# Kernel tuning notes

Measured on AMD Instinct MI355X. Metric: run time of the kernel, lower is better.

Reference implementation:

```python
import jax, jax.numpy as jnp
import numpy as np

D = 768        # word_emb_dim * 3 (span embedding dim)
H = 1024       # assumed FFNNScore hidden width
K = 250        # antecedent window (self.k)
P_LAMBDA = 0.4


def setup_inputs() -> dict:
    key = jax.random.key(0)
    ks = jax.random.split(key, 8)
    N, T = 2000, 1000
    return {
        "vectors": jax.random.normal(ks[0], (N, D), jnp.float32),
        "Wm1": jax.random.normal(ks[1], (D, H), jnp.float32) / np.sqrt(D),
        "bm1": jnp.zeros((H,), jnp.float32),
        "wm2": jax.random.normal(ks[2], (H,), jnp.float32) / np.sqrt(H),
        "bm2": jnp.zeros((1,), jnp.float32),
        "Wp1": jax.random.normal(ks[3], (3 * D, H), jnp.float32) / np.sqrt(3 * D),
        "bp1": jnp.zeros((H,), jnp.float32),
        "wp2": jax.random.normal(ks[4], (H,), jnp.float32) / np.sqrt(H),
        "bp2": jnp.zeros((1,), jnp.float32),
        "span_starts": jax.random.randint(ks[5], (N,), 0, T, dtype=jnp.int32),
        "span_ends": jax.random.randint(ks[6], (N,), 0, T, dtype=jnp.int32),
        "t": T,
    }


def reference(vectors, Wm1, bm1, wm2, bm2, Wp1, bp1, wp2, bp2,
              span_starts, span_ends, t):
    m = int(P_LAMBDA * t)  # number of retained spans (static)

    # mention scorer: FFNN over all span embeddings  [N]
    scores = jax.nn.relu(vectors @ Wm1 + bm1) @ wm2 + bm2[0]

    # prune to top int(p_lambda * t) spans by mention score (descending sort)
    top = jnp.argsort(-scores)[:m]
    s_top, v_top = scores[top], vectors[top]

    # re-sort retained spans by (i_start, i_end) descending
    order = jnp.lexsort((span_ends[top], span_starts[top]))[::-1]
    v, s = v_top[order], s_top[order]  # [m, D], [m]

    # pairwise scorer weight split for cat([a, b, a*b]) @ Wp1
    Wa, Wb, Wab = Wp1[:D], Wp1[D:2 * D], Wp1[2 * D:]

    # antecedent windows: span i vs spans i+1 .. i+K (padded/masked)
    idx = jnp.arange(m - 1)[:, None] + 1 + jnp.arange(K)[None, :]  # [m-1, K]
    valid = idx < m
    idxc = jnp.minimum(idx, m - 1)

    a = v[:m - 1]                      # [m-1, D]
    b = v[idxc]                        # [m-1, K, D]
    hb = (v @ Wb)[idxc]                # gather precomputed b-projection [m-1, K, H]
    h = jax.nn.relu((a @ Wa)[:, None, :] + hb
                    + jnp.einsum('ikd,dh->ikh', a[:, None, :] * b, Wab)
                    + bp1)             # [m-1, K, H]
    pairwise = h @ wp2 + bp2[0]        # [m-1, K]

    ant = pairwise + s[idxc] + s[:m - 1, None]
    ant = jnp.where(valid, ant, -jnp.inf)
    # dummy antecedent (epsilon) score 0 appended, then softmax per span
    full = jnp.concatenate([ant, jnp.zeros((m - 1, 1), ant.dtype)], axis=1)
    return jax.nn.softmax(full, axis=-1)  # [m-1, K+1]
```

## Files before the change

### kernel.cpp

```cpp
#include <hip/hip_runtime.h>
#include <hip/hip_bf16.h>
#include <math.h>

#define NVEC 2000
#define DD   768
#define HH   1024
#define KNUM 250
#define MSEL 400
#define MR   399
#define OUTW 251
#define PPAD 256
#define NPAIR (MR * PPAD)
#define BM 128
#define BN 256
#define BK 64
#define NKT (DD / BK)
#define NNB (HH / BN)

typedef short  bf16x8 __attribute__((ext_vector_type(8)));
typedef float  f32x4  __attribute__((ext_vector_type(4)));
typedef unsigned int u32;
typedef u32    u32x4  __attribute__((ext_vector_type(4)));

__device__ __forceinline__ float waveSum(float p) {
#pragma unroll
  for (int off = 32; off >= 1; off >>= 1) p += __shfl_xor(p, off, 64);
  return p;
}
__device__ __forceinline__ float waveMax(float p) {
#pragma unroll
  for (int off = 32; off >= 1; off >>= 1) p = fmaxf(p, __shfl_xor(p, off, 64));
  return p;
}
__device__ __forceinline__ short f2bf(float f) {
  __hip_bfloat16 h = __float2bfloat16(f);
  return __builtin_bit_cast(short, h);
}
__device__ __forceinline__ void gload_lds16(const void* g, void* l) {
  __builtin_amdgcn_global_load_lds(
      (const __attribute__((address_space(1))) u32*)g,
      (__attribute__((address_space(3))) u32*)l, 16, 0, 0);
}
__device__ __forceinline__ bf16x8 prodcvt(const float* av, bf16x8 b) {
  u32x4 u = __builtin_bit_cast(u32x4, b);
  bf16x8 r;
#pragma unroll
  for (int p = 0; p < 4; ++p) {
    const float blo = __builtin_bit_cast(float, u[p] << 16);
    const float bhi = __builtin_bit_cast(float, u[p] & 0xffff0000u);
    r[2 * p]     = f2bf(av[2 * p]     * blo);
    r[2 * p + 1] = f2bf(av[2 * p + 1] * bhi);
  }
  return r;
}

__global__ __launch_bounds__(512) void scores_kernel(
    const float* __restrict__ vectors, const float* __restrict__ Wm1,
    const float* __restrict__ bm1, const float* __restrict__ wm2,
    const float* __restrict__ bm2, float* __restrict__ scores) {
  __shared__ float vrow[8 * DD];
  __shared__ float red[8];
  const int tid = threadIdx.x;
  const int base = blockIdx.x * 8;
  for (int idx = tid; idx < 8 * DD; idx += 512)
    vrow[idx] = vectors[base * DD + idx];
  __syncthreads();
  float acc[8][2];
#pragma unroll
  for (int r = 0; r < 8; ++r) { acc[r][0] = 0.f; acc[r][1] = 0.f; }
#pragma unroll 4
  for (int d = 0; d < DD; ++d) {
    const float2 w = ((const float2*)(Wm1 + (size_t)d * HH))[tid];
#pragma unroll
    for (int r = 0; r < 8; ++r) {
      const float a = vrow[r * DD + d];
      acc[r][0] += a * w.x; acc[r][1] += a * w.y;
    }
  }
  const float2 b = ((const float2*)bm1)[tid];
  const float2 m = ((const float2*)wm2)[tid];
  const float sc = bm2[0];
  for (int r = 0; r < 8; ++r) {
    float p = fmaxf(acc[r][0] + b.x, 0.f) * m.x + fmaxf(acc[r][1] + b.y, 0.f) * m.y;
    p = waveSum(p);
    if ((tid & 63) == 0) red[tid >> 6] = p;
    __syncthreads();
    if (tid == 0) {
      float t = red[0];
#pragma unroll
      for (int w8 = 1; w8 < 8; ++w8) t += red[w8];
      scores[base + r] = t + sc;
    }
    __syncthreads();
  }
}

__global__ __launch_bounds__(1024) void topsort_kernel(
    const float* __restrict__ scores, int* __restrict__ top) {
  __shared__ float ks[2048];
  __shared__ int   ki[2048];
  const int tid = threadIdx.x;
  for (int e = tid; e < 2048; e += 1024) {
    ks[e] = (e < NVEC) ? scores[e] : -INFINITY;
    ki[e] = e;
  }
  __syncthreads();
  for (int k = 2; k <= 2048; k <<= 1) {
    for (int j = k >> 1; j > 0; j >>= 1) {
      for (int e = tid; e < 2048; e += 1024) {
        const int l = e ^ j;
        if (l > e) {
          const float s1 = ks[e], s2 = ks[l];
          const int i1 = ki[e], i2 = ki[l];
          const bool first = (s1 > s2) || (s1 == s2 && i1 < i2);
          const bool up = ((e & k) == 0);
          if (up ? !first : first) {
            ks[e] = s2; ks[l] = s1; ki[e] = i2; ki[l] = i1;
          }
        }
      }
      __syncthreads();
    }
  }
  if (tid < MSEL) top[tid] = ki[tid];
}

__global__ __launch_bounds__(256) void lexsort_kernel(
    const int* __restrict__ top, const int* __restrict__ sst,
    const int* __restrict__ sen, const float* __restrict__ scores,
    int* __restrict__ perm, float* __restrict__ sfin) {
  __shared__ int s_st[512], s_en[512], s_j[512];
  const int tid = threadIdx.x;
  for (int e = tid; e < 512; e += 256) {
    if (e < MSEL) { const int ti = top[e]; s_st[e] = sst[ti]; s_en[e] = sen[ti]; }
    else { s_st[e] = 0x7fffffff; s_en[e] = 0x7fffffff; }
    s_j[e] = e;
  }
  __syncthreads();
  for (int k = 2; k <= 512; k <<= 1) {
    for (int j = k >> 1; j > 0; j >>= 1) {
      for (int e = tid; e < 512; e += 256) {
        const int l = e ^ j;
        if (l > e) {
          const int a0 = s_st[e], a1 = s_en[e], a2 = s_j[e];
          const int b0 = s_st[l], b1 = s_en[l], b2 = s_j[l];
          const bool first = (a0 < b0) || (a0 == b0 && (a1 < b1 || (a1 == b1 && a2 < b2)));
          const bool up = ((e & k) == 0);
          if (up ? !first : first) {
            s_st[e] = b0; s_en[e] = b1; s_j[e] = b2;
            s_st[l] = a0; s_en[l] = a1; s_j[l] = a2;
          }
        }
      }
      __syncthreads();
    }
  }
  for (int i = tid; i < MSEL; i += 256) {
    const int src = s_j[MSEL - 1 - i];
    const int vi = top[src];
    perm[i] = vi;
    sfin[i] = scores[vi];
  }
}

__global__ __launch_bounds__(256) void hab_kernel(
    const float* __restrict__ vectors, const float* __restrict__ Wp1,
    const int* __restrict__ perm, float* __restrict__ Ha, float* __restrict__ Hv,
    float* __restrict__ Vp, ushort* __restrict__ Vpb) {
  __shared__ float vrow[8 * DD];
  const int tid = threadIdx.x;
  const int base = blockIdx.x * 8;
  const int mat = blockIdx.y >> 1;
  const int half = blockIdx.y & 1;
  for (int r = 0; r < 8; ++r) {
    const int pi = perm[base + r];
    for (int d = tid; d < DD; d += 256) {
      const float val = vectors[pi * DD + d];
      vrow[r * DD + d] = val;
      if (blockIdx.y == 0) {
        Vp[(size_t)(base + r) * DD + d] = val;
        Vpb[(size_t)(base + r) * DD + d] = (ushort)f2bf(val);
      }
    }
  }
  __syncthreads();
  float acc[8][2];
#pragma unroll
  for (int r = 0; r < 8; ++r) { acc[r][0] = 0.f; acc[r][1] = 0.f; }
  const float* W = Wp1 + (size_t)mat * DD * HH + half * 512;
#pragma unroll 4
  for (int d = 0; d < DD; ++d) {
    const float2 w = ((const float2*)(W + (size_t)d * HH))[tid];
#pragma unroll
    for (int r = 0; r < 8; ++r) {
      const float a = vrow[r * DD + d];
      acc[r][0] += a * w.x; acc[r][1] += a * w.y;
    }
  }
  float* dst = mat ? Hv : Ha;
  for (int r = 0; r < 8; ++r) {
    const int row = base + r;
    if (mat == 0 && row >= MR) continue;
    ((float2*)(dst + (size_t)row * HH + half * 512))[tid] =
        make_float2(acc[r][0], acc[r][1]);
  }
}

__global__ __launch_bounds__(256) void wt_kernel(
    const float* __restrict__ Wp1, ushort* __restrict__ Wt) {
  __shared__ float tile[64][65];
  const int kb = blockIdx.x;
  const int nb = blockIdx.y;
  const float* Wab = Wp1 + 2 * DD * HH;
  for (int idx = threadIdx.x; idx < 64 * 64; idx += 256) {
    const int kk = idx >> 6, nn = idx & 63;
    tile[kk][nn] = Wab[(size_t)(kb * 64 + kk) * HH + nb * 64 + nn];
  }
  __syncthreads();
  for (int idx = threadIdx.x; idx < 64 * 64; idx += 256) {
    const int nn = idx >> 6, kk = idx & 63;
    Wt[(size_t)(nb * 64 + nn) * DD + kb * 64 + kk] = (ushort)f2bf(tile[kk][nn]);
  }
}

__global__ __launch_bounds__(512, 2) void pair_kernel(
    const float* __restrict__ Vp, const ushort* __restrict__ Vpb,
    const ushort* __restrict__ Wt,
    const float* __restrict__ bp1, const float* __restrict__ wp2,
    const float* __restrict__ Ha, const float* __restrict__ Hv,
    float* __restrict__ pp) {
  __shared__ __align__(16) ushort As[BM * BK];
  __shared__ __align__(16) ushort Bs[BN * BK];
  __shared__ float redp[BM][4];
  const int tid = threadIdx.x;
  const int mb = blockIdx.x;
  const int nb = blockIdx.y;
  const int i = mb >> 1;
  const int khalf = mb & 1;
  const int n0 = nb * BN;
  const int lane = tid & 63;
  const int wid = tid >> 6;
  const int wr = wid >> 2, wc = wid & 3;
  const int lhi = lane >> 4, llo = lane & 15;

  const int cs = tid & 7;
  const int rb9 = tid >> 3;
  const int csx = cs ^ (rb9 & 7);
  const ushort* vsrc[2];
  int rowA[2];
#pragma unroll
  for (int it = 0; it < 2; ++it) {
    rowA[it] = it * 64 + rb9;
    int j = i + 1 + khalf * BM + rowA[it];
    if (j > MR) j = MR;
    vsrc[it] = Vpb + (size_t)j * DD + cs * 8;
  }
  int rowB[4];
#pragma unroll
  for (int it = 0; it < 4; ++it) rowB[it] = it * 64 + rb9;
  const float* avp = Vp + (size_t)i * DD + cs * 8;

  f32x4 acc[4][4];
#pragma unroll
  for (int a = 0; a < 4; ++a)
#pragma unroll
    for (int b = 0; b < 4; ++b) acc[a][b] = (f32x4){0.f, 0.f, 0.f, 0.f};

  for (int kt = 0; kt < NKT; ++kt) {
    const int kg = kt * BK;
    bf16x8 bv[2];
    float av[8];
#pragma unroll
    for (int it = 0; it < 2; ++it) bv[it] = *(const bf16x8*)(vsrc[it] + kg);
    *(float4*)(av) = *(const float4*)(avp + kg);
    *(float4*)(av + 4) = *(const float4*)(avp + kg + 4);
#pragma unroll
    for (int it = 0; it < 4; ++it)
      gload_lds16(Wt + (size_t)(n0 + rowB[it]) * DD + kg + csx * 8,
                  (char*)Bs + (it * 512 + tid) * 16);
#pragma unroll
    for (int it = 0; it < 2; ++it)
      *(bf16x8*)((char*)As + rowA[it] * 128 + (csx << 4)) = prodcvt(av, bv[it]);
    __syncthreads();
#pragma unroll
    for (int ks = 0; ks < 2; ++ks) {
      bf16x8 af[4], bfr[4];
#pragma unroll
      for (int mi = 0; mi < 4; ++mi) {
        const int row = wr * 64 + mi * 16 + llo;
        const int ch = (ks * 4 + lhi) ^ (row & 7);
        af[mi] = *(const bf16x8*)((const char*)As + row * 128 + (ch << 4));
      }
#pragma unroll
      for (int ni = 0; ni < 4; ++ni) {
        const int row = wc * 64 + ni * 16 + llo;
        const int ch = (ks * 4 + lhi) ^ (row & 7);
        bfr[ni] = *(const bf16x8*)((const char*)Bs + row * 128 + (ch << 4));
      }
#pragma unroll
      for (int mi = 0; mi < 4; ++mi)
#pragma unroll
        for (int ni = 0; ni < 4; ++ni)
          acc[mi][ni] = __builtin_amdgcn_mfma_f32_16x16x32_bf16(af[mi], bfr[ni], acc[mi][ni], 0, 0, 0);
    }
    __syncthreads();
  }

  float hb4[4], wpv[4];
  int cg[4];
#pragma unroll
  for (int ni = 0; ni < 4; ++ni) {
    const int col = n0 + wc * 64 + ni * 16 + llo;
    cg[ni] = col;
    hb4[ni] = Ha[(size_t)i * HH + col] + bp1[col];
    wpv[ni] = wp2[col];
  }
#pragma unroll
  for (int mi = 0; mi < 4; ++mi) {
#pragma unroll
    for (int r = 0; r < 4; ++r) {
      const int rowl = wr * 64 + mi * 16 + lhi * 4 + r;
      int j = i + 1 + khalf * BM + rowl;
      if (j > MR) j = MR;
      float part = 0.f;
#pragma unroll
      for (int ni = 0; ni < 4; ++ni) {
        const float pre = acc[mi][ni][r] + hb4[ni] + Hv[(size_t)j * HH + cg[ni]];
        part += fmaxf(pre, 0.f) * wpv[ni];
      }
      part += __shfl_xor(part, 1, 64);
      part += __shfl_xor(part, 2, 64);
      part += __shfl_xor(part, 4, 64);
      part += __shfl_xor(part, 8, 64);
      if (llo == 0) redp[rowl][wc] = part;
    }
  }
  __syncthreads();
  if (tid < BM)
    pp[(size_t)nb * NPAIR + (size_t)i * PPAD + khalf * BM + tid] =
        redp[tid][0] + redp[tid][1] + redp[tid][2] + redp[tid][3];
}

__global__ __launch_bounds__(256) void softmax_kernel(
    const float* __restrict__ pp, const float* __restrict__ sfin,
    const float* __restrict__ bp2, float* __restrict__ out) {
  __shared__ float red[4];
  const int i = blockIdx.x, tid = threadIdx.x;
  float v;
  if (tid < KNUM) {
    const int jidx = i + 1 + tid;
    const bool valid = jidx < MSEL;
    const int jc = valid ? jidx : MR;
    float s = 0.f;
#pragma unroll
    for (int b = 0; b < NNB; ++b) s += pp[(size_t)b * NPAIR + i * PPAD + tid];
    v = valid ? (s + bp2[0] + sfin[jc] + sfin[i]) : -INFINITY;
  } else if (tid == KNUM) v = 0.f;
  else v = -INFINITY;
  float mx = waveMax(v);
  if ((tid & 63) == 0) red[tid >> 6] = mx;
  __syncthreads();
  const float m = fmaxf(fmaxf(red[0], red[1]), fmaxf(red[2], red[3]));
  __syncthreads();
  const float e = (tid <= KNUM) ? expf(v - m) : 0.f;
  float s = waveSum(e);
  if ((tid & 63) == 0) red[tid >> 6] = s;
  __syncthreads();
  const float tot = red[0] + red[1] + red[2] + red[3];
  if (tid <= KNUM) out[i * OUTW + tid] = e / tot;
}

extern "C" void kernel_launch(void* const* d_in, const int* in_sizes, int n_in,
                              void* d_out, int out_size, void* d_ws, size_t ws_size,
                              hipStream_t stream) {
  const float* vectors = (const float*)d_in[0];
  const float* Wm1 = (const float*)d_in[1];
  const float* bm1 = (const float*)d_in[2];
  const float* wm2 = (const float*)d_in[3];
  const float* bm2 = (const float*)d_in[4];
  const float* Wp1 = (const float*)d_in[5];
  const float* bp1 = (const float*)d_in[6];
  const float* wp2 = (const float*)d_in[7];
  const float* bp2 = (const float*)d_in[8];
  const int* sst = (const int*)d_in[9];
  const int* sen = (const int*)d_in[10];
  float* out = (float*)d_out;
  char* ws = (char*)d_ws;

  float* scores = (float*)(ws);
  int*   top    = (int*)(ws + 8192);
  int*   perm   = (int*)(ws + 10240);
  float* sfin   = (float*)(ws + 12288);
  float* Ha     = (float*)(ws + 16384);
  float* Hv     = (float*)(ws + 16384 + 1638400);
  float* Vp     = (float*)(ws + 3293184);
  ushort* Wt    = (ushort*)(ws + 4521984);
  ushort* Vpb   = (ushort*)(ws + 6094848);
  float* pp     = (float*)(ws + 6709248);

  scores_kernel<<<NVEC / 8, 512, 0, stream>>>(vectors, Wm1, bm1, wm2, bm2, scores);
  topsort_kernel<<<1, 1024, 0, stream>>>(scores, top);
  lexsort_kernel<<<1, 256, 0, stream>>>(top, sst, sen, scores, perm, sfin);
  wt_kernel<<<dim3(12, 16), 256, 0, stream>>>(Wp1, Wt);
  hab_kernel<<<dim3(MSEL / 8, 4), 256, 0, stream>>>(vectors, Wp1, perm, Ha, Hv, Vp, Vpb);
  pair_kernel<<<dim3(MR * 2, NNB), 512, 0, stream>>>(Vp, Vpb, Wt, bp1, wp2, Ha, Hv, pp);
  softmax_kernel<<<MR, 256, 0, stream>>>(pp, sfin, bp2, out);
}
```

Measured before the change: 405.5 us.

## Prepack Wab into MFMA fragment layout and load B directly into registers

```diff
diff --git a/kernel.cpp b/kernel.cpp
--- a/kernel.cpp
+++ b/kernel.cpp
@@ -16,6 +16,7 @@
 #define BK 64
 #define NKT (DD / BK)
 #define NNB (HH / BN)
+#define NKQ (DD / 32)
 
 typedef short  bf16x8 __attribute__((ext_vector_type(8)));
 typedef float  f32x4  __attribute__((ext_vector_type(4)));
@@ -35,11 +36,6 @@
 __device__ __forceinline__ short f2bf(float f) {
   __hip_bfloat16 h = __float2bfloat16(f);
   return __builtin_bit_cast(short, h);
-}
-__device__ __forceinline__ void gload_lds16(const void* g, void* l) {
-  __builtin_amdgcn_global_load_lds(
-      (const __attribute__((address_space(1))) u32*)g,
-      (__attribute__((address_space(3))) u32*)l, 16, 0, 0);
 }
 __device__ __forceinline__ bf16x8 prodcvt(const float* av, bf16x8 b) {
   u32x4 u = __builtin_bit_cast(u32x4, b);
@@ -95,10 +91,13 @@
   }
 }
 
-__global__ __launch_bounds__(1024) void topsort_kernel(
-    const float* __restrict__ scores, int* __restrict__ top) {
+__global__ __launch_bounds__(1024) void sort_kernel(
+    const float* __restrict__ scores, const int* __restrict__ sst,
+    const int* __restrict__ sen, int* __restrict__ perm,
+    float* __restrict__ sfin) {
   __shared__ float ks[2048];
   __shared__ int   ki[2048];
+  __shared__ int s_st[512], s_en[512], s_j[512];
   const int tid = threadIdx.x;
   for (int e = tid; e < 2048; e += 1024) {
     ks[e] = (e < NVEC) ? scores[e] : -INFINITY;
@@ -122,24 +121,15 @@
       __syncthreads();
     }
   }
-  if (tid < MSEL) top[tid] = ki[tid];
-}
-
-__global__ __launch_bounds__(256) void lexsort_kernel(
-    const int* __restrict__ top, const int* __restrict__ sst,
-    const int* __restrict__ sen, const float* __restrict__ scores,
-    int* __restrict__ perm, float* __restrict__ sfin) {
-  __shared__ int s_st[512], s_en[512], s_j[512];
-  const int tid = threadIdx.x;
-  for (int e = tid; e < 512; e += 256) {
-    if (e < MSEL) { const int ti = top[e]; s_st[e] = sst[ti]; s_en[e] = sen[ti]; }
+  for (int e = tid; e < 512; e += 1024) {
+    if (e < MSEL) { const int ti = ki[e]; s_st[e] = sst[ti]; s_en[e] = sen[ti]; }
     else { s_st[e] = 0x7fffffff; s_en[e] = 0x7fffffff; }
     s_j[e] = e;
   }
   __syncthreads();
   for (int k = 2; k <= 512; k <<= 1) {
     for (int j = k >> 1; j > 0; j >>= 1) {
-      for (int e = tid; e < 512; e += 256) {
+      for (int e = tid; e < 512; e += 1024) {
         const int l = e ^ j;
         if (l > e) {
           const int a0 = s_st[e], a1 = s_en[e], a2 = s_j[e];
@@ -155,9 +145,9 @@
       __syncthreads();
     }
   }
-  for (int i = tid; i < MSEL; i += 256) {
+  for (int i = tid; i < MSEL; i += 1024) {
     const int src = s_j[MSEL - 1 - i];
-    const int vi = top[src];
+    const int vi = ki[src];
     perm[i] = vi;
     sfin[i] = scores[vi];
   }
@@ -206,8 +196,8 @@
   }
 }
 
-__global__ __launch_bounds__(256) void wt_kernel(
-    const float* __restrict__ Wp1, ushort* __restrict__ Wt) {
+__global__ __launch_bounds__(256) void wt2_kernel(
+    const float* __restrict__ Wp1, ushort* __restrict__ Wt2) {
   __shared__ float tile[64][65];
   const int kb = blockIdx.x;
   const int nb = blockIdx.y;
@@ -217,20 +207,28 @@
     tile[kk][nn] = Wab[(size_t)(kb * 64 + kk) * HH + nb * 64 + nn];
   }
   __syncthreads();
-  for (int idx = threadIdx.x; idx < 64 * 64; idx += 256) {
-    const int nn = idx >> 6, kk = idx & 63;
-    Wt[(size_t)(nb * 64 + nn) * DD + kb * 64 + kk] = (ushort)f2bf(tile[kk][nn]);
+  for (int c = threadIdx.x; c < 512; c += 256) {
+    const int lane = c & 63;
+    const int sub = c >> 6;
+    const int ntl = sub >> 1, kql = sub & 1;
+    const int llo = lane & 15, lhi = lane >> 4;
+    const int nt = nb * 4 + ntl;
+    const int kq = kb * 2 + kql;
+    bf16x8 v;
+#pragma unroll
+    for (int e = 0; e < 8; ++e)
+      v[e] = f2bf(tile[kql * 32 + lhi * 8 + e][ntl * 16 + llo]);
+    *(bf16x8*)(Wt2 + ((size_t)(nt * NKQ + kq) * 64 + lane) * 8) = v;
   }
 }
 
 __global__ __launch_bounds__(512, 2) void pair_kernel(
     const float* __restrict__ Vp, const ushort* __restrict__ Vpb,
-    const ushort* __restrict__ Wt,
+    const ushort* __restrict__ Wt2,
     const float* __restrict__ bp1, const float* __restrict__ wp2,
     const float* __restrict__ Ha, const float* __restrict__ Hv,
     float* __restrict__ pp) {
   __shared__ __align__(16) ushort As[BM * BK];
-  __shared__ __align__(16) ushort Bs[BN * BK];
   __shared__ float redp[BM][4];
   const int tid = threadIdx.x;
   const int mb = blockIdx.x;
@@ -255,10 +253,9 @@
     if (j > MR) j = MR;
     vsrc[it] = Vpb + (size_t)j * DD + cs * 8;
   }
-  int rowB[4];
-#pragma unroll
-  for (int it = 0; it < 4; ++it) rowB[it] = it * 64 + rb9;
   const float* avp = Vp + (size_t)i * DD + cs * 8;
+
+  const ushort* wt2base = Wt2 + ((size_t)((n0 >> 4) + wc * 4) * NKQ) * 512 + lane * 8;
 
   f32x4 acc[4][4];
 #pragma unroll
@@ -275,34 +272,39 @@
     *(float4*)(av) = *(const float4*)(avp + kg);
     *(float4*)(av + 4) = *(const float4*)(avp + kg + 4);
 #pragma unroll
-    for (int it = 0; it < 4; ++it)
-      gload_lds16(Wt + (size_t)(n0 + rowB[it]) * DD + kg + csx * 8,
-                  (char*)Bs + (it * 512 + tid) * 16);
-#pragma unroll
     for (int it = 0; it < 2; ++it)
       *(bf16x8*)((char*)As + rowA[it] * 128 + (csx << 4)) = prodcvt(av, bv[it]);
     __syncthreads();
-#pragma unroll
-    for (int ks = 0; ks < 2; ++ks) {
-      bf16x8 af[4], bfr[4];
-#pragma unroll
-      for (int mi = 0; mi < 4; ++mi) {
-        const int row = wr * 64 + mi * 16 + llo;
-        const int ch = (ks * 4 + lhi) ^ (row & 7);
-        af[mi] = *(const bf16x8*)((const char*)As + row * 128 + (ch << 4));
-      }
-#pragma unroll
-      for (int ni = 0; ni < 4; ++ni) {
-        const int row = wc * 64 + ni * 16 + llo;
-        const int ch = (ks * 4 + lhi) ^ (row & 7);
-        bfr[ni] = *(const bf16x8*)((const char*)Bs + row * 128 + (ch << 4));
-      }
-#pragma unroll
-      for (int mi = 0; mi < 4; ++mi)
-#pragma unroll
-        for (int ni = 0; ni < 4; ++ni)
-          acc[mi][ni] = __builtin_amdgcn_mfma_f32_16x16x32_bf16(af[mi], bfr[ni], acc[mi][ni], 0, 0, 0);
-    }
+    bf16x8 bfr0[4], bfr1[4];
+#pragma unroll
+    for (int ni = 0; ni < 4; ++ni)
+      bfr0[ni] = *(const bf16x8*)(wt2base + (ni * NKQ + kt * 2 + 0) * 512);
+#pragma unroll
+    for (int ni = 0; ni < 4; ++ni)
+      bfr1[ni] = *(const bf16x8*)(wt2base + (ni * NKQ + kt * 2 + 1) * 512);
+    bf16x8 af[4];
+#pragma unroll
+    for (int mi = 0; mi < 4; ++mi) {
+      const int row = wr * 64 + mi * 16 + llo;
+      const int ch = lhi ^ (row & 7);
+      af[mi] = *(const bf16x8*)((const char*)As + row * 128 + (ch << 4));
+    }
+#pragma unroll
+    for (int mi = 0; mi < 4; ++mi)
+#pragma unroll
+      for (int ni = 0; ni < 4; ++ni)
+        acc[mi][ni] = __builtin_amdgcn_mfma_f32_16x16x32_bf16(af[mi], bfr0[ni], acc[mi][ni], 0, 0, 0);
+#pragma unroll
+    for (int mi = 0; mi < 4; ++mi) {
+      const int row = wr * 64 + mi * 16 + llo;
+      const int ch = (4 + lhi) ^ (row & 7);
+      af[mi] = *(const bf16x8*)((const char*)As + row * 128 + (ch << 4));
+    }
+#pragma unroll
+    for (int mi = 0; mi < 4; ++mi)
+#pragma unroll
+      for (int ni = 0; ni < 4; ++ni)
+        acc[mi][ni] = __builtin_amdgcn_mfma_f32_16x16x32_bf16(af[mi], bfr1[ni], acc[mi][ni], 0, 0, 0);
     __syncthreads();
   }
 
@@ -388,21 +390,19 @@
   char* ws = (char*)d_ws;
 
   float* scores = (float*)(ws);
-  int*   top    = (int*)(ws + 8192);
   int*   perm   = (int*)(ws + 10240);
   float* sfin   = (float*)(ws + 12288);
   float* Ha     = (float*)(ws + 16384);
   float* Hv     = (float*)(ws + 16384 + 1638400);
   float* Vp     = (float*)(ws + 3293184);
-  ushort* Wt    = (ushort*)(ws + 4521984);
+  ushort* Wt2   = (ushort*)(ws + 4521984);
   ushort* Vpb   = (ushort*)(ws + 6094848);
   float* pp     = (float*)(ws + 6709248);
 
   scores_kernel<<<NVEC / 8, 512, 0, stream>>>(vectors, Wm1, bm1, wm2, bm2, scores);
-  topsort_kernel<<<1, 1024, 0, stream>>>(scores, top);
-  lexsort_kernel<<<1, 256, 0, stream>>>(top, sst, sen, scores, perm, sfin);
-  wt_kernel<<<dim3(12, 16), 256, 0, stream>>>(Wp1, Wt);
+  sort_kernel<<<1, 1024, 0, stream>>>(scores, sst, sen, perm, sfin);
+  wt2_kernel<<<dim3(12, 16), 256, 0, stream>>>(Wp1, Wt2);
   hab_kernel<<<dim3(MSEL / 8, 4), 256, 0, stream>>>(vectors, Wp1, perm, Ha, Hv, Vp, Vpb);
-  pair_kernel<<<dim3(MR * 2, NNB), 512, 0, stream>>>(Vp, Vpb, Wt, bp1, wp2, Ha, Hv, pp);
+  pair_kernel<<<dim3(MR * 2, NNB), 512, 0, stream>>>(Vp, Vpb, Wt2, bp1, wp2, Ha, Hv, pp);
   softmax_kernel<<<MR, 256, 0, stream>>>(pp, sfin, bp2, out);
 }
```

Measured after the change: 400.8 us. No clear change (-1.2%).
